# Kernel tuning notes

Hardware: AMD Instinct MI355X
Metric: run time of the kernel (lower is better)

## Reference

```python
import jax, jax.numpy as jnp
import numpy as np

NUM_HEADS = 64
NUM_HEADS_KV = 1
HEAD_SIZE = 64
HIDDEN = NUM_HEADS * HEAD_SIZE  # 4096
SOFTMAX_SCALE = HEAD_SIZE ** -0.5
BATCH = 4
SEQ = 1024
TOTAL = BATCH * SEQ


def setup_inputs() -> dict:
    key = jax.random.key(0)
    k1, k2, k3, k4, k5 = jax.random.split(key, 5)
    hidden_states = jax.random.normal(k1, (TOTAL, HIDDEN), dtype=jnp.float32)
    # rotary cos/sin per token position (head_size/2 features, rotate-half style)
    pos = jnp.tile(jnp.arange(SEQ, dtype=jnp.float32), BATCH)  # [TOTAL]
    inv_freq = 1.0 / (10000.0 ** (jnp.arange(0, HEAD_SIZE, 2, dtype=jnp.float32) / HEAD_SIZE))
    freqs = pos[:, None] * inv_freq[None, :]  # [TOTAL, 32]
    cos = jnp.cos(freqs)
    sin = jnp.sin(freqs)
    w_qkv = jax.random.normal(k2, (HIDDEN, HIDDEN + 2 * NUM_HEADS_KV * HEAD_SIZE), dtype=jnp.float32) * (HIDDEN ** -0.5)
    w_dense = jax.random.normal(k3, (HIDDEN, HIDDEN), dtype=jnp.float32) * (HIDDEN ** -0.5)
    cu_seqlen_prefill = jnp.arange(BATCH + 1, dtype=jnp.int32) * SEQ
    return {
        "hidden_states": hidden_states,
        "cos": cos,
        "sin": sin,
        "w_qkv": w_qkv,
        "w_dense": w_dense,
        "cu_seqlen_prefill": cu_seqlen_prefill,
    }


def _rope(x, cos, sin):
    # x: [T, H, D]; cos/sin: [T, D/2]; rotate-half pairing (x1=first half, x2=second half)
    d2 = x.shape[-1] // 2
    x1, x2 = x[..., :d2], x[..., d2:]
    c = cos[:, None, :]
    s = sin[:, None, :]
    return jnp.concatenate([x1 * c - x2 * s, x2 * c + x1 * s], axis=-1)


def reference(hidden_states, cos, sin, w_qkv, w_dense, cu_seqlen_prefill):
    T = hidden_states.shape[0]
    B = cu_seqlen_prefill.shape[0] - 1
    S = T // B
    qkv = hidden_states @ w_qkv  # [T, H*D + 2*D]
    q = qkv[:, : NUM_HEADS * HEAD_SIZE].reshape(T, NUM_HEADS, HEAD_SIZE)
    kv = qkv[:, NUM_HEADS * HEAD_SIZE:].reshape(T, 2, NUM_HEADS_KV, HEAD_SIZE)
    k = kv[:, 0]  # [T, 1, D]
    v = kv[:, 1]
    q = _rope(q, cos, sin)
    k = _rope(k, cos, sin)
    # ragged sequences of equal length -> batch view (prefill flash-attn path, causal)
    qb = q.reshape(B, S, NUM_HEADS, HEAD_SIZE)
    kb = k.reshape(B, S, NUM_HEADS_KV, HEAD_SIZE)[:, :, 0]  # MQA: single kv head [B,S,D]
    vb = v.reshape(B, S, NUM_HEADS_KV, HEAD_SIZE)[:, :, 0]
    scores = jnp.einsum("bshd,btd->bhst", qb, kb) * SOFTMAX_SCALE  # [B,H,S,S]
    causal = jnp.tril(jnp.ones((S, S), dtype=bool))
    scores = jnp.where(causal[None, None], scores, jnp.finfo(scores.dtype).min)
    p = jax.nn.softmax(scores, axis=-1)
    out = jnp.einsum("bhst,btd->bshd", p, vb)  # [B,S,H,D]
    out = out.reshape(T, NUM_HEADS * HEAD_SIZE)
    return out @ w_dense
```

## Files before the change

### kernel.cpp

```cpp
#include <hip/hip_runtime.h>
#include <hip/hip_bf16.h>
#include <stdint.h>

#define HID   4096
#define NQKV  4224
#define TOT   4096
#define SEQq  1024
#define NH    64
#define HD    64
#define SM_SCALE 0.125f
#define LOG2E 1.44269504088896f

typedef float  f32x4  __attribute__((ext_vector_type(4)));
typedef short  short8 __attribute__((ext_vector_type(8)));
typedef ushort ushort4v __attribute__((ext_vector_type(4)));
typedef uint32_t uint2v __attribute__((ext_vector_type(2)));

static __device__ __forceinline__ ushort f2bf(float f) {
    uint32_t u = __float_as_uint(f);
    u += 0x7FFFu + ((u >> 16) & 1u);
    return (ushort)(u >> 16);
}

static __device__ __forceinline__ uint32_t cvt_pk_bf16(float lo, float hi) {
    uint32_t r;
    asm("v_cvt_pk_bf16_f32 %0, %1, %2" : "=v"(r) : "v"(lo), "v"(hi));
    return r;
}

static __device__ __forceinline__ void gload_lds16(const void* g, void* l) {
    __builtin_amdgcn_global_load_lds(
        (const __attribute__((address_space(1))) uint32_t*)g,
        (__attribute__((address_space(3))) uint32_t*)l, 16, 0, 0);
}

__global__ __launch_bounds__(256) void cast_bf16_kernel(
    const float* __restrict__ in, ushort* __restrict__ out, int n4)
{
    int i = blockIdx.x * 256 + threadIdx.x;
    if (i < n4) {
        float4 v = ((const float4*)in)[i];
        ushort4v o;
        o.x = f2bf(v.x); o.y = f2bf(v.y); o.z = f2bf(v.z); o.w = f2bf(v.w);
        ((ushort4v*)out)[i] = o;
    }
}

__global__ __launch_bounds__(256) void transpose_cast_kernel(
    const float* __restrict__ in, ushort* __restrict__ out, int R, int C)
{
    __shared__ float tile[32][33];
    int c0 = blockIdx.x * 32, r0 = blockIdx.y * 32;
    int tx = threadIdx.x & 31, ty = threadIdx.x >> 5;
#pragma unroll
    for (int i = 0; i < 4; i++)
        tile[ty + i * 8][tx] = in[(size_t)(r0 + ty + i * 8) * C + c0 + tx];
    __syncthreads();
#pragma unroll
    for (int i = 0; i < 4; i++)
        out[(size_t)(c0 + ty + i * 8) * R + r0 + tx] = f2bf(tile[tx][ty + i * 8]);
}

#define BUFSZ 49152
template<int EPI>
__global__ __launch_bounds__(512, 1) void gemm2_kernel(
    const ushort* __restrict__ A, const ushort* __restrict__ B,
    float* __restrict__ Cf, ushort* __restrict__ qkv, ushort* __restrict__ vt,
    const float* __restrict__ cosT, const float* __restrict__ sinT,
    int M, int N, int K, int MB)
{
    extern __shared__ char lds[];
    const int tid = threadIdx.x;
    const int lane = tid & 63, wave = tid >> 6;
    const int wm = wave >> 1, wn = wave & 1;

    const int nwg = gridDim.x;
    const int cpx = nwg >> 3;
    const int id2 = (blockIdx.x & 7) * cpx + (blockIdx.x >> 3);
    const int by = id2 % MB, bx = id2 / MB;
    const int m0 = by * 256, n0 = bx * 128;

    f32x4 acc[4][4] = {};

    const int srow = tid >> 3;
    const int scw  = ((tid & 7) ^ (srow & 7)) << 3;
    const ushort* Abase = A + (size_t)m0 * K;
    const ushort* Bbase = B + (size_t)n0 * K;
    const int NT = K >> 6;

#define STAGE(t)  {                                                          \
        char* buf = lds + ((t) % 3) * BUFSZ;                                 \
        const int k0 = (t) << 6;                                             \
        _Pragma("unroll")                                                    \
        for (int a = 0; a < 4; a++)                                          \
            gload_lds16(Abase + (size_t)(a * 64 + srow) * K + k0 + scw,      \
                        buf + a * 8192 + wave * 1024);                       \
        _Pragma("unroll")                                                    \
        for (int b2 = 0; b2 < 2; b2++)                                       \
            gload_lds16(Bbase + (size_t)(b2 * 64 + srow) * K + k0 + scw,     \
                        buf + 32768 + b2 * 8192 + wave * 1024);              \
    }

    STAGE(0);
    STAGE(1);

    for (int t = 0; t < NT; t++) {
        if (t + 1 < NT)
            asm volatile("s_waitcnt vmcnt(6)" ::: "memory");
        else
            asm volatile("s_waitcnt vmcnt(0)" ::: "memory");
        __builtin_amdgcn_s_barrier();
        asm volatile("" ::: "memory");
        if (t + 2 < NT) STAGE(t + 2);

        const char* bufA = lds + (t % 3) * BUFSZ;
        const char* bufB = bufA + 32768;
        short8 af[4][2], bfr[4][2];
#pragma unroll
        for (int ks = 0; ks < 2; ks++) {
            const int cb = (ks * 64 + ((lane >> 4) << 4)) ^ ((lane & 7) << 4);
#pragma unroll
            for (int m = 0; m < 4; m++)
                af[m][ks] = *(const short8*)(bufA +
                    (wm * 64 + m * 16 + (lane & 15)) * 128 + cb);
#pragma unroll
            for (int n = 0; n < 4; n++)
                bfr[n][ks] = *(const short8*)(bufB +
                    (wn * 64 + n * 16 + (lane & 15)) * 128 + cb);
        }
        __builtin_amdgcn_s_setprio(1);
#pragma unroll
        for (int ks = 0; ks < 2; ks++)
#pragma unroll
            for (int m = 0; m < 4; m++)
#pragma unroll
                for (int n = 0; n < 4; n++)
                    acc[m][n] = __builtin_amdgcn_mfma_f32_16x16x32_bf16(
                        af[m][ks], bfr[n][ks], acc[m][n], 0, 0, 0);
        __builtin_amdgcn_s_setprio(0);
    }
#undef STAGE

    if (EPI == 0) {
#pragma unroll
        for (int m = 0; m < 4; m++) {
            int row = m0 + wm * 64 + m * 16 + ((lane >> 4) << 2);
#pragma unroll
            for (int n = 0; n < 4; n++) {
                int col = n0 + wn * 64 + n * 16 + (lane & 15);
#pragma unroll
                for (int j = 0; j < 4; j++)
                    Cf[(size_t)(row + j) * N + col] = acc[m][n][j];
            }
        }
    } else {
        const int cn = n0 + wn * 64;
        if (cn < HID + HD) {
#pragma unroll
            for (int m = 0; m < 4; m++)
#pragma unroll
                for (int j = 0; j < 4; j++) {
                    int t = m0 + wm * 64 + m * 16 + ((lane >> 4) << 2) + j;
#pragma unroll
                    for (int n = 0; n < 2; n++) {
                        int d = n * 16 + (lane & 15);
                        float c = cosT[t * 32 + d];
                        float s = sinT[t * 32 + d];
                        float x1 = acc[m][n][j], x2 = acc[m][n + 2][j];
                        qkv[(size_t)t * NQKV + cn + d]      = f2bf(x1 * c - x2 * s);
                        qkv[(size_t)t * NQKV + cn + d + 32] = f2bf(x2 * c + x1 * s);
                    }
                }
        } else {
#pragma unroll
            for (int m = 0; m < 4; m++)
#pragma unroll
                for (int n = 0; n < 4; n++)
#pragma unroll
                    for (int j = 0; j < 4; j++) {
                        int t = m0 + wm * 64 + m * 16 + ((lane >> 4) << 2) + j;
                        int d = n * 16 + (lane & 15);
                        vt[(size_t)((t >> 10) * 64 + d) * SEQq + (t & 1023)] =
                            f2bf(acc[m][n][j]);
                    }
        }
    }
}

__global__ __launch_bounds__(256, 4) void attn_kernel(
    const ushort* __restrict__ qkv, const ushort* __restrict__ vt,
    ushort* __restrict__ aout)
{
    __shared__ char plds[16384];
    const int lane = threadIdx.x & 63, wave = threadIdx.x >> 6;
    const int h = blockIdx.y, b = blockIdx.z;
    char* pbase = plds + wave * 4096;
    const int l15 = lane & 15, lg = lane >> 4;
    const float Cs = SM_SCALE * LOG2E;

    for (int pass = 0; pass < 2; pass++) {
        const int qt = (pass == 0) ? blockIdx.x : 7 - blockIdx.x;
        const int q0 = qt * 128 + wave * 32;

        short8 aq[2][2];
#pragma unroll
        for (int n = 0; n < 2; n++)
#pragma unroll
            for (int ks = 0; ks < 2; ks++)
                aq[n][ks] = *(const short8*)(qkv +
                    (size_t)(b * SEQq + q0 + n * 16 + l15) * NQKV +
                    h * HD + ks * 32 + lg * 8);

        f32x4 oT[4][2] = {};
        float Lp[2] = {};
        const int nfull = q0 >> 6;

        for (int t = 0; t <= nfull; t++) {
            const int kv0 = t << 6;
            const bool diag = (t == nfull);
            const int mh = diag ? ((q0 & 32) ? 4 : 2) : 4;

            f32x4 scT[4][2] = {};
#pragma unroll
            for (int ks = 0; ks < 2; ks++) {
                short8 bk[4];
                for (int m = 0; m < mh; m++)
                    bk[m] = *(const short8*)(qkv +
                        (size_t)(b * SEQq + kv0 + m * 16 + l15) * NQKV +
                        HID + ks * 32 + lg * 8);
                for (int m = 0; m < mh; m++)
#pragma unroll
                    for (int n = 0; n < 2; n++)
                        scT[m][n] = __builtin_amdgcn_mfma_f32_16x16x32_bf16(
                            bk[m], aq[n][ks], scT[m][n], 0, 0, 0);
            }

            for (int m = 0; m < mh; m++)
#pragma unroll
                for (int n = 0; n < 2; n++) {
                    float p4[4];
#pragma unroll
                    for (int j = 0; j < 4; j++) {
                        float e = __builtin_amdgcn_exp2f(scT[m][n][j] * Cs);
                        if (diag) {
                            int kvg = kv0 + m * 16 + lg * 4 + j;
                            int qg  = q0 + n * 16 + l15;
                            e = (kvg <= qg) ? e : 0.f;
                        }
                        Lp[n] += e;
                        p4[j] = e;
                    }
                    uint2v pk;
                    pk.x = cvt_pk_bf16(p4[0], p4[1]);
                    pk.y = cvt_pk_bf16(p4[2], p4[3]);
                    int q = n * 16 + l15;
                    int kb = m * 32 + lg * 8;
                    *(uint2v*)(pbase + q * 128 +
                               ((((kb >> 4) ^ (q & 7)) << 4) | (kb & 15))) = pk;
                }

            for (int ks2 = 0; ks2 < (mh >> 1); ks2++) {
                short8 vb[4], pb[2];
#pragma unroll
                for (int md = 0; md < 4; md++)
                    vb[md] = *(const short8*)(vt +
                        (size_t)(b * 64 + md * 16 + l15) * SEQq +
                        kv0 + ks2 * 32 + lg * 8);
#pragma unroll
                for (int no = 0; no < 2; no++) {
                    int q = no * 16 + l15;
                    pb[no] = *(const short8*)(pbase + q * 128 +
                        (((ks2 * 4 + lg) ^ (q & 7)) << 4));
                }
#pragma unroll
                for (int md = 0; md < 4; md++)
#pragma unroll
                    for (int no = 0; no < 2; no++)
                        oT[md][no] = __builtin_amdgcn_mfma_f32_16x16x32_bf16(
                            vb[md], pb[no], oT[md][no], 0, 0, 0);
            }
        }

        float inv[2];
#pragma unroll
        for (int no = 0; no < 2; no++) {
            float L = Lp[no];
            L += __shfl_xor(L, 16);
            L += __shfl_xor(L, 32);
            inv[no] = 1.f / L;
        }
#pragma unroll
        for (int md = 0; md < 4; md++)
#pragma unroll
            for (int no = 0; no < 2; no++) {
                uint2v s;
                s.x = cvt_pk_bf16(oT[md][no][0] * inv[no], oT[md][no][1] * inv[no]);
                s.y = cvt_pk_bf16(oT[md][no][2] * inv[no], oT[md][no][3] * inv[no]);
                int tq = b * SEQq + q0 + no * 16 + l15;
                *(uint2v*)(aout + (size_t)tq * HID + h * HD + md * 16 + lg * 4) = s;
            }
    }
}

extern "C" void kernel_launch(void* const* d_in, const int* in_sizes, int n_in,
                              void* d_out, int out_size, void* d_ws, size_t ws_size,
                              hipStream_t stream)
{
    const float* hidden  = (const float*)d_in[0];
    const float* cosT    = (const float*)d_in[1];
    const float* sinT    = (const float*)d_in[2];
    const float* w_qkv   = (const float*)d_in[3];
    const float* w_dense = (const float*)d_in[4];
    float* out = (float*)d_out;

    char* ws = (char*)d_ws;
    ushort* hB   = (ushort*)(ws);
    ushort* wqT  = (ushort*)(ws + 33554432);
    ushort* wdT  = (ushort*)(ws + 68157440);
    ushort* qkvB = (ushort*)(ws + 101711872);
    ushort* vtB  = (ushort*)(ws + 136314880);
    ushort* aoB  = (ushort*)(ws + 136839168);

    hipFuncSetAttribute((const void*)gemm2_kernel<1>,
                        hipFuncAttributeMaxDynamicSharedMemorySize, 3 * BUFSZ);
    hipFuncSetAttribute((const void*)gemm2_kernel<0>,
                        hipFuncAttributeMaxDynamicSharedMemorySize, 3 * BUFSZ);

    cast_bf16_kernel<<<16384, 256, 0, stream>>>(hidden, hB, TOT * HID / 4);
    transpose_cast_kernel<<<dim3(NQKV / 32, HID / 32), 256, 0, stream>>>(
        w_qkv, wqT, HID, NQKV);
    transpose_cast_kernel<<<dim3(HID / 32, HID / 32), 256, 0, stream>>>(
        w_dense, wdT, HID, HID);
    gemm2_kernel<1><<<528, 512, 3 * BUFSZ, stream>>>(
        hB, wqT, nullptr, qkvB, vtB, cosT, sinT, TOT, NQKV, HID, TOT / 256);
    attn_kernel<<<dim3(4, NH, 4), 256, 0, stream>>>(qkvB, vtB, aoB);
    gemm2_kernel<0><<<512, 512, 3 * BUFSZ, stream>>>(
        aoB, wdT, out, nullptr, nullptr, nullptr, nullptr, TOT, HID, HID, TOT / 256);
}
```

Baseline: 764.1 us.

## Fold softmax scale into Q, compute row sums via MFMA, restructure attention grid

The softmax scale times log2(e) is folded into the Q projection epilogue so the attention loop skips a multiply per score. The row-sum of probabilities is now accumulated with an extra MFMA against a ones vector, which replaces the per-element adds and the cross-lane shuffles. The grid doubles to one q-tile per block instead of two balanced passes, with launch bounds raised to 6 for occupancy and setprio around the PV MFMAs. Outputs are staged through LDS for coalesced 16-byte stores. Dropping the paired passes loses causal load balancing, and Q is now rounded to bf16 after scaling.

```diff
diff --git a/kernel.cpp b/kernel.cpp
--- a/kernel.cpp
+++ b/kernel.cpp
@@ -156,6 +156,7 @@
     } else {
         const int cn = n0 + wn * 64;
         if (cn < HID + HD) {
+            const float sc = (cn < HID) ? (SM_SCALE * LOG2E) : 1.0f;
 #pragma unroll
             for (int m = 0; m < 4; m++)
 #pragma unroll
@@ -167,8 +168,8 @@
                         float c = cosT[t * 32 + d];
                         float s = sinT[t * 32 + d];
                         float x1 = acc[m][n][j], x2 = acc[m][n + 2][j];
-                        qkv[(size_t)t * NQKV + cn + d]      = f2bf(x1 * c - x2 * s);
-                        qkv[(size_t)t * NQKV + cn + d + 32] = f2bf(x2 * c + x1 * s);
+                        qkv[(size_t)t * NQKV + cn + d]      = f2bf((x1 * c - x2 * s) * sc);
+                        qkv[(size_t)t * NQKV + cn + d + 32] = f2bf((x2 * c + x1 * s) * sc);
                     }
                 }
         } else {
@@ -187,7 +188,7 @@
     }
 }
 
-__global__ __launch_bounds__(256, 4) void attn_kernel(
+__global__ __launch_bounds__(256, 6) void attn_kernel(
     const ushort* __restrict__ qkv, const ushort* __restrict__ vt,
     ushort* __restrict__ aout)
 {
@@ -196,109 +197,120 @@
     const int h = blockIdx.y, b = blockIdx.z;
     char* pbase = plds + wave * 4096;
     const int l15 = lane & 15, lg = lane >> 4;
-    const float Cs = SM_SCALE * LOG2E;
-
-    for (int pass = 0; pass < 2; pass++) {
-        const int qt = (pass == 0) ? blockIdx.x : 7 - blockIdx.x;
-        const int q0 = qt * 128 + wave * 32;
-
-        short8 aq[2][2];
-#pragma unroll
-        for (int n = 0; n < 2; n++)
-#pragma unroll
-            for (int ks = 0; ks < 2; ks++)
-                aq[n][ks] = *(const short8*)(qkv +
-                    (size_t)(b * SEQq + q0 + n * 16 + l15) * NQKV +
-                    h * HD + ks * 32 + lg * 8);
-
-        f32x4 oT[4][2] = {};
-        float Lp[2] = {};
-        const int nfull = q0 >> 6;
-
-        for (int t = 0; t <= nfull; t++) {
-            const int kv0 = t << 6;
-            const bool diag = (t == nfull);
-            const int mh = diag ? ((q0 & 32) ? 4 : 2) : 4;
-
-            f32x4 scT[4][2] = {};
-#pragma unroll
-            for (int ks = 0; ks < 2; ks++) {
-                short8 bk[4];
-                for (int m = 0; m < mh; m++)
-                    bk[m] = *(const short8*)(qkv +
-                        (size_t)(b * SEQq + kv0 + m * 16 + l15) * NQKV +
-                        HID + ks * 32 + lg * 8);
-                for (int m = 0; m < mh; m++)
-#pragma unroll
-                    for (int n = 0; n < 2; n++)
-                        scT[m][n] = __builtin_amdgcn_mfma_f32_16x16x32_bf16(
-                            bk[m], aq[n][ks], scT[m][n], 0, 0, 0);
+
+    short8 ones;
+#pragma unroll
+    for (int i = 0; i < 8; i++) ones[i] = (short)0x3F80;
+
+    const int qt = blockIdx.x;
+    const int q0 = qt * 128 + wave * 32;
+
+    short8 aq[2][2];
+#pragma unroll
+    for (int n = 0; n < 2; n++)
+#pragma unroll
+        for (int ks = 0; ks < 2; ks++)
+            aq[n][ks] = *(const short8*)(qkv +
+                (size_t)(b * SEQq + q0 + n * 16 + l15) * NQKV +
+                h * HD + ks * 32 + lg * 8);
+
+    f32x4 oT[5][2] = {};
+    const int nfull = q0 >> 6;
+
+    for (int t = 0; t <= nfull; t++) {
+        const int kv0 = t << 6;
+        const bool diag = (t == nfull);
+        const int mh = diag ? ((q0 & 32) ? 4 : 2) : 4;
+
+        f32x4 scT[4][2] = {};
+#pragma unroll
+        for (int ks = 0; ks < 2; ks++) {
+            short8 bk[4];
+            for (int m = 0; m < mh; m++)
+                bk[m] = *(const short8*)(qkv +
+                    (size_t)(b * SEQq + kv0 + m * 16 + l15) * NQKV +
+                    HID + ks * 32 + lg * 8);
+            for (int m = 0; m < mh; m++)
+#pragma unroll
+                for (int n = 0; n < 2; n++)
+                    scT[m][n] = __builtin_amdgcn_mfma_f32_16x16x32_bf16(
+                        bk[m], aq[n][ks], scT[m][n], 0, 0, 0);
+        }
+
+        for (int m = 0; m < mh; m++)
+#pragma unroll
+            for (int n = 0; n < 2; n++) {
+                float p4[4];
+#pragma unroll
+                for (int j = 0; j < 4; j++) {
+                    float e = __builtin_amdgcn_exp2f(scT[m][n][j]);
+                    if (diag) {
+                        int kvg = kv0 + m * 16 + lg * 4 + j;
+                        int qg  = q0 + n * 16 + l15;
+                        e = (kvg <= qg) ? e : 0.f;
+                    }
+                    p4[j] = e;
+                }
+                uint2v pk;
+                pk.x = cvt_pk_bf16(p4[0], p4[1]);
+                pk.y = cvt_pk_bf16(p4[2], p4[3]);
+                int q = n * 16 + l15;
+                int kb = m * 32 + lg * 8;
+                *(uint2v*)(pbase + q * 128 +
+                           ((((kb >> 4) ^ (q & 7)) << 4) | (kb & 15))) = pk;
             }
 
-            for (int m = 0; m < mh; m++)
-#pragma unroll
-                for (int n = 0; n < 2; n++) {
-                    float p4[4];
-#pragma unroll
-                    for (int j = 0; j < 4; j++) {
-                        float e = __builtin_amdgcn_exp2f(scT[m][n][j] * Cs);
-                        if (diag) {
-                            int kvg = kv0 + m * 16 + lg * 4 + j;
-                            int qg  = q0 + n * 16 + l15;
-                            e = (kvg <= qg) ? e : 0.f;
-                        }
-                        Lp[n] += e;
-                        p4[j] = e;
-                    }
-                    uint2v pk;
-                    pk.x = cvt_pk_bf16(p4[0], p4[1]);
-                    pk.y = cvt_pk_bf16(p4[2], p4[3]);
-                    int q = n * 16 + l15;
-                    int kb = m * 32 + lg * 8;
-                    *(uint2v*)(pbase + q * 128 +
-                               ((((kb >> 4) ^ (q & 7)) << 4) | (kb & 15))) = pk;
-                }
-
-            for (int ks2 = 0; ks2 < (mh >> 1); ks2++) {
-                short8 vb[4], pb[2];
-#pragma unroll
-                for (int md = 0; md < 4; md++)
-                    vb[md] = *(const short8*)(vt +
-                        (size_t)(b * 64 + md * 16 + l15) * SEQq +
-                        kv0 + ks2 * 32 + lg * 8);
-#pragma unroll
-                for (int no = 0; no < 2; no++) {
-                    int q = no * 16 + l15;
-                    pb[no] = *(const short8*)(pbase + q * 128 +
-                        (((ks2 * 4 + lg) ^ (q & 7)) << 4));
-                }
-#pragma unroll
-                for (int md = 0; md < 4; md++)
-#pragma unroll
-                    for (int no = 0; no < 2; no++)
-                        oT[md][no] = __builtin_amdgcn_mfma_f32_16x16x32_bf16(
-                            vb[md], pb[no], oT[md][no], 0, 0, 0);
+        for (int ks2 = 0; ks2 < (mh >> 1); ks2++) {
+            short8 vb[4], pb[2];
+#pragma unroll
+            for (int md = 0; md < 4; md++)
+                vb[md] = *(const short8*)(vt +
+                    (size_t)(b * 64 + md * 16 + l15) * SEQq +
+                    kv0 + ks2 * 32 + lg * 8);
+#pragma unroll
+            for (int no = 0; no < 2; no++) {
+                int q = no * 16 + l15;
+                pb[no] = *(const short8*)(pbase + q * 128 +
+                    (((ks2 * 4 + lg) ^ (q & 7)) << 4));
             }
-        }
-
-        float inv[2];
+            __builtin_amdgcn_s_setprio(1);
+#pragma unroll
+            for (int md = 0; md < 4; md++)
+#pragma unroll
+                for (int no = 0; no < 2; no++)
+                    oT[md][no] = __builtin_amdgcn_mfma_f32_16x16x32_bf16(
+                        vb[md], pb[no], oT[md][no], 0, 0, 0);
+#pragma unroll
+            for (int no = 0; no < 2; no++)
+                oT[4][no] = __builtin_amdgcn_mfma_f32_16x16x32_bf16(
+                    ones, pb[no], oT[4][no], 0, 0, 0);
+            __builtin_amdgcn_s_setprio(0);
+        }
+    }
+
+    float inv[2];
+#pragma unroll
+    for (int no = 0; no < 2; no++)
+        inv[no] = 1.f / oT[4][no][0];
+#pragma unroll
+    for (int md = 0; md < 4; md++)
 #pragma unroll
         for (int no = 0; no < 2; no++) {
-            float L = Lp[no];
-            L += __shfl_xor(L, 16);
-            L += __shfl_xor(L, 32);
-            inv[no] = 1.f / L;
-        }
-#pragma unroll
-        for (int md = 0; md < 4; md++)
-#pragma unroll
-            for (int no = 0; no < 2; no++) {
-                uint2v s;
-                s.x = cvt_pk_bf16(oT[md][no][0] * inv[no], oT[md][no][1] * inv[no]);
-                s.y = cvt_pk_bf16(oT[md][no][2] * inv[no], oT[md][no][3] * inv[no]);
-                int tq = b * SEQq + q0 + no * 16 + l15;
-                *(uint2v*)(aout + (size_t)tq * HID + h * HD + md * 16 + lg * 4) = s;
-            }
+            uint2v s;
+            s.x = cvt_pk_bf16(oT[md][no][0] * inv[no], oT[md][no][1] * inv[no]);
+            s.y = cvt_pk_bf16(oT[md][no][2] * inv[no], oT[md][no][3] * inv[no]);
+            int q = no * 16 + l15;
+            int kb = md * 32 + lg * 8;
+            *(uint2v*)(pbase + q * 128 +
+                       ((((kb >> 4) ^ (q & 7)) << 4) | (kb & 15))) = s;
+        }
+#pragma unroll
+    for (int i = 0; i < 4; i++) {
+        int q = i * 8 + (lane >> 3);
+        short8 v = *(const short8*)(pbase + q * 128 +
+                                    (((lane & 7) ^ (q & 7)) << 4));
+        int tq = b * SEQq + q0 + q;
+        *(short8*)(aout + (size_t)tq * HID + h * HD + (lane & 7) * 8) = v;
     }
 }
 
@@ -333,7 +345,7 @@
         w_dense, wdT, HID, HID);
     gemm2_kernel<1><<<528, 512, 3 * BUFSZ, stream>>>(
         hB, wqT, nullptr, qkvB, vtB, cosT, sinT, TOT, NQKV, HID, TOT / 256);
-    attn_kernel<<<dim3(4, NH, 4), 256, 0, stream>>>(qkvB, vtB, aoB);
+    attn_kernel<<<dim3(8, NH, 4), 256, 0, stream>>>(qkvB, vtB, aoB);
     gemm2_kernel<0><<<512, 512, 3 * BUFSZ, stream>>>(
         aoB, wdT, out, nullptr, nullptr, nullptr, nullptr, TOT, HID, HID, TOT / 256);
 }
```

Result: slower. 1.826 ms (+139.0%).
